# Kernel optimization log

Measured on AMD Instinct MI355X. Metric: run time of the kernel, lower is better.

The kernel has to match this reference:

```python
import jax, jax.numpy as jnp
import numpy as np

N = 50000
EPS = 1e-5


def _layernorm(x, g, b):
    mu = jnp.mean(x, axis=-1, keepdims=True)
    var = jnp.mean((x - mu) ** 2, axis=-1, keepdims=True)
    return (x - mu) * jax.lax.rsqrt(var + EPS) * g + b


def _gcn_conv(x, W, b, src, dst, norm, n):
    # PyG GCNConv: x' = D^{-1/2}(A+I)D^{-1/2} (x W) + b, self-loops already in src/dst
    xw = x @ W                                   # [N, F_out]
    msg = xw[src] * norm[:, None]                # gather + scale, [E+N, F_out]
    return jax.ops.segment_sum(msg, dst, num_segments=n) + b


def _prep_edges(edge_index, n):
    loops = jnp.arange(n, dtype=edge_index.dtype)
    src = jnp.concatenate([edge_index[0], loops])
    dst = jnp.concatenate([edge_index[1], loops])
    deg = jax.ops.segment_sum(jnp.ones(dst.shape[0], jnp.float32), dst, num_segments=n)
    dinv = jnp.where(deg > 0, jax.lax.rsqrt(deg), 0.0)
    norm = dinv[src] * dinv[dst]
    return src, dst, norm


def setup_inputs() -> dict:
    key = jax.random.key(0)
    ks = jax.random.split(key, 8)
    gene, hid, nc = 512, 256, 4
    x = jax.random.normal(ks[0], (N, gene), jnp.float32)
    edge_index = jax.random.randint(ks[1], (2, 1600000), 0, N, dtype=jnp.int64)

    def lin(k, fi, fo):
        return jax.random.normal(k, (fi, fo), jnp.float32) / np.sqrt(fi)

    d = {
        "x": x, "edge_index": edge_index,
        "W1": lin(ks[2], gene, hid), "b1": jnp.zeros(hid, jnp.float32),
        "W2": lin(ks[3], hid, 2 * hid), "b2": jnp.zeros(2 * hid, jnp.float32),
        "W3": lin(ks[4], 2 * hid, hid), "b3": jnp.zeros(hid, jnp.float32),
        "W4": lin(ks[5], hid, hid // 2), "b4": jnp.zeros(hid // 2, jnp.float32),
        "Wc": lin(ks[6], hid // 2, nc), "bc": jnp.zeros(nc, jnp.float32),
        "g1": jnp.ones(hid, jnp.float32), "be1": jnp.zeros(hid, jnp.float32),
        "g2": jnp.ones(2 * hid, jnp.float32), "be2": jnp.zeros(2 * hid, jnp.float32),
        "g3": jnp.ones(hid, jnp.float32), "be3": jnp.zeros(hid, jnp.float32),
        "g4": jnp.ones(hid // 2, jnp.float32), "be4": jnp.zeros(hid // 2, jnp.float32),
    }
    return d


def reference(x, edge_index, W1, b1, W2, b2, W3, b3, W4, b4, Wc, bc,
              g1, be1, g2, be2, g3, be3, g4, be4):
    n = x.shape[0]
    src, dst, norm = _prep_edges(edge_index, n)
    # dropout layers are identity (training=False)
    h1 = jax.nn.elu(_layernorm(_gcn_conv(x, W1, b1, src, dst, norm, n), g1, be1))
    h2 = jax.nn.elu(_layernorm(_gcn_conv(h1, W2, b2, src, dst, norm, n), g2, be2))
    h3 = jax.nn.elu(_layernorm(_gcn_conv(h2, W3, b3, src, dst, norm, n), g3, be3))
    h4_in = h3 + h1
    out_conv = _gcn_conv(h4_in, W4, b4, src, dst, norm, n)
    out_bn = _layernorm(out_conv, g4, be4)
    h = jax.nn.elu(out_bn)
    return (h @ Wc + bc, out_conv, out_bn)
```

## Files before the change

### kernel.cpp

```cpp
#include <hip/hip_runtime.h>
#include <hip/hip_bf16.h>
#include <math.h>

typedef unsigned short u16;
typedef u16 us8 __attribute__((ext_vector_type(8)));
typedef u16 us4 __attribute__((ext_vector_type(4)));
typedef float f32x4 __attribute__((ext_vector_type(4)));
typedef float f32x8 __attribute__((ext_vector_type(8)));
typedef __bf16 bf8 __attribute__((ext_vector_type(8)));

#define SCAN_B 256
#define CH 8192

__device__ __forceinline__ float bf2f(u16 v) {
    unsigned u = ((unsigned)v) << 16;
    return __builtin_bit_cast(float, u);
}
__device__ __forceinline__ u16 f2bf(float f) {
    unsigned u = __builtin_bit_cast(unsigned, f);
    unsigned lsb = (u >> 16) & 1;
    u += 0x7fff + lsb;
    return (u16)(u >> 16);
}
__device__ __forceinline__ void fma8(f32x8& acc, float w, us8 v) {
#pragma unroll
    for (int j = 0; j < 8; j++) acc[j] += w * bf2f(v[j]);
}

__global__ void detect_k(const int* __restrict__ ei, int E,
                         const u16* __restrict__ xraw, int* flag) {
    __shared__ int c_i32, c_f32;
    if (threadIdx.x == 0) { c_i32 = 0; c_f32 = 0; }
    __syncthreads();
    int ne = (E < 4096) ? E : 4096;
    for (int e = threadIdx.x; e < ne; e += blockDim.x)
        if (ei[2 * e + 1] != 0) c_i32 = 1;
    for (int k = threadIdx.x; k < 8192; k += blockDim.x) {
        u16 v = xraw[2 * k];
        int ex = (v >> 7) & 0xFF;
        if (ex >= 0xF0) atomicAdd(&c_f32, 1);
    }
    __syncthreads();
    if (threadIdx.x == 0) {
        flag[0] = (c_i32 == 0) ? 1 : 0;
        flag[1] = (c_f32 >= 4) ? 1 : 0;
    }
}

struct WEnt { const void* s; u16* dst; int K; int Nn; int base; };
struct PEnt { const void* s; int n; int off; };
struct PTab { PEnt e[14]; };

#define GX_CVT 4096

__global__ void megacvt_k(const void* __restrict__ xsrc, u16* __restrict__ xdst,
                          long nq, WEnt e0, WEnt e1, WEnt e2, WEnt e3, int wtotal,
                          PTab tab, float* __restrict__ pbuf,
                          const int* __restrict__ flag, int gw) {
    int f32m = flag[1];
    int bid = blockIdx.x;
    if (bid < GX_CVT) {
        long i0 = (long)bid * blockDim.x + threadIdx.x;
        long stride = (long)GX_CVT * blockDim.x;
        if (f32m) {
            const f32x4* s = (const f32x4*)xsrc;
            for (long i = i0; i < nq; i += stride) {
                f32x4 v = s[i];
                us4 o;
                #pragma unroll
                for (int j = 0; j < 4; j++) o[j] = f2bf(v[j]);
                ((us4*)xdst)[i] = o;
            }
        } else {
            const us4* s = (const us4*)xsrc;
            for (long i = i0; i < nq; i += stride) ((us4*)xdst)[i] = s[i];
        }
    } else if (bid < GX_CVT + gw) {
        int t = (bid - GX_CVT) * blockDim.x + threadIdx.x;
        if (t >= wtotal) return;
        WEnt en = (t >= e3.base) ? e3 : ((t >= e2.base) ? e2 : ((t >= e1.base) ? e1 : e0));
        int li = t - en.base;
        int k = li / en.Nn, nn = li - k * en.Nn;
        u16 b;
        if (f32m) b = f2bf(((const float*)en.s)[li]);
        else      b = ((const u16*)en.s)[li];
        en.dst[nn * en.K + k] = b;
    } else {
        PEnt en = tab.e[bid - GX_CVT - gw];
        for (int i = threadIdx.x; i < en.n; i += blockDim.x) {
            float v = f32m ? ((const float*)en.s)[i] : bf2f(((const u16*)en.s)[i]);
            pbuf[en.off + i] = v;
        }
    }
}

__global__ void histA_k(const int* __restrict__ ei, const int* __restrict__ flag,
                        int* __restrict__ hist, int* __restrict__ counts,
                        int E, int n, int NB, int NBUK, int shiftv) {
    __shared__ int lh[256];
    int blk = blockIdx.x;
    int gi = blk * 256 + threadIdx.x;
    if (gi < n) counts[gi] = 1;
    for (int b = threadIdx.x; b < NBUK; b += 256) lh[b] = 0;
    __syncthreads();
    int e0 = blk * CH;
    int e1 = min(e0 + CH, E);
    int i64 = flag[0];
    for (int e = e0 + threadIdx.x; e < e1; e += 256) {
        int d;
        if (i64) d = (int)((const long long*)ei)[(size_t)E + e];
        else     d = ei[(size_t)E + e];
        int b = ((unsigned)d < (unsigned)n) ? min(d >> shiftv, NBUK - 1) : (NBUK - 1);
        atomicAdd(&lh[b], 1);
    }
    __syncthreads();
    for (int b = threadIdx.x; b < NBUK; b += 256) hist[b * NB + blk] = lh[b];
}

__global__ void scan1_k(const int* __restrict__ counts, int* incl, int* bsum, int n) {
    __shared__ int tmp[SCAN_B];
    int t = threadIdx.x;
    int i = blockIdx.x * SCAN_B + t;
    int v = (i < n) ? counts[i] : 0;
    tmp[t] = v;
    __syncthreads();
    for (int o = 1; o < SCAN_B; o <<= 1) {
        int x = 0;
        if (t >= o) x = tmp[t - o];
        __syncthreads();
        if (t >= o) tmp[t] += x;
        __syncthreads();
    }
    if (i < n) incl[i] = tmp[t];
    if (t == SCAN_B - 1) bsum[blockIdx.x] = tmp[t];
}

__global__ void scan2_k(const int* __restrict__ bsum, int* bscan, int nb) {
    __shared__ int tmp[SCAN_B];
    int t = threadIdx.x;
    tmp[t] = (t < nb) ? bsum[t] : 0;
    __syncthreads();
    for (int o = 1; o < SCAN_B; o <<= 1) {
        int x = 0;
        if (t >= o) x = tmp[t - o];
        __syncthreads();
        if (t >= o) tmp[t] += x;
        __syncthreads();
    }
    bscan[t] = tmp[t];
}

__global__ void scatC_k(const int* __restrict__ ei, const int* __restrict__ flag,
                        const int* __restrict__ histincl, const int* __restrict__ bscan,
                        const int* __restrict__ hist, long long* __restrict__ ebuf,
                        int* __restrict__ counts,
                        int E, int n, int NB, int NBUK, int shiftv) {
    __shared__ int cur[256];
    int blk = blockIdx.x;
    for (int b = threadIdx.x; b < NBUK; b += 256) {
        int fi = b * NB + blk;
        int boff = (fi >= 256) ? bscan[(fi >> 8) - 1] : 0;
        cur[b] = histincl[fi] + boff - hist[fi];
    }
    __syncthreads();
    int e0 = blk * CH;
    int e1 = min(e0 + CH, E);
    int i64 = flag[0];
    for (int e = e0 + threadIdx.x; e < e1; e += 256) {
        int s, d;
        if (i64) {
            const long long* e64 = (const long long*)ei;
            s = (int)e64[e]; d = (int)e64[(size_t)E + e];
        } else {
            s = ei[e]; d = ei[(size_t)E + e];
        }
        int b = ((unsigned)d < (unsigned)n) ? min(d >> shiftv, NBUK - 1) : (NBUK - 1);
        int pos = atomicAdd(&cur[b], 1);
        ebuf[pos] = ((long long)(unsigned)d << 32) | (unsigned)s;
        if ((unsigned)d < (unsigned)n) atomicAdd(&counts[d], 1);
    }
}

__global__ void finCSR_k(const int* __restrict__ incl, const int* __restrict__ bscan,
                         const int* __restrict__ counts, int* __restrict__ rowptr,
                         int* __restrict__ cursor, float* __restrict__ dinv, int n) {
    int i = blockIdx.x * SCAN_B + threadIdx.x;
    if (i < n) {
        int boff = (blockIdx.x > 0) ? bscan[blockIdx.x - 1] : 0;
        int rp_end = incl[i] + boff;
        rowptr[i + 1] = rp_end;
        if (i == 0) rowptr[0] = 0;
        cursor[i] = rp_end - counts[i];
        dinv[i] = rsqrtf((float)counts[i]);
    }
}

__global__ void scatD_k(const long long* __restrict__ ebuf, int* cursor,
                        int* __restrict__ col, int E, int n) {
    int e = blockIdx.x * blockDim.x + threadIdx.x;
    if (e < E) {
        long long pr = ebuf[e];
        int d = (int)(pr >> 32);
        int s = (int)(pr & 0xffffffffLL);
        if ((unsigned)s < (unsigned)n && (unsigned)d < (unsigned)n) {
            int pos = atomicAdd(&cursor[d], 1);
            col[pos] = s;
        }
    } else if (e < E + n) {
        int i = e - E;
        int pos = atomicAdd(&cursor[i], 1);
        col[pos] = i;
    }
}

typedef __attribute__((address_space(1))) const void gas_v;
typedef __attribute__((address_space(3))) void las_v;

__global__ __launch_bounds__(256) void gemm128_k(
    const u16* __restrict__ A, const u16* __restrict__ Bt,
    u16* __restrict__ C, int M, int K, int Nn, int nyv) {
    int nx = (M + 127) >> 7;
    int nfull = nx & ~7;
    int cutoff = nfull * nyv;
    int b = blockIdx.x;
    int bx, by;
    if (b < cutoff) {
        int k = b & 7;
        int q = b >> 3;
        by = q % nyv;
        bx = (q / nyv) * 8 + k;
    } else {
        int r = b - cutoff;
        bx = nfull + r / nyv;
        by = r % nyv;
    }

    __shared__ u16 As[2][128 * 32];
    __shared__ u16 Bs[2][128 * 32];
    int tid = threadIdx.x;
    int wave = tid >> 6;
    int lane = tid & 63;
    int wr = (wave >> 1) * 64;
    int wc = (wave & 1) * 64;
    long row0 = (long)bx * 128;
    int col0 = by * 128;
    int lr = lane >> 2;
    int lc = lane & 3;
    int m = lane & 15;
    int q = lane >> 4;

    long ar0 = row0 + (wave + 0) * 16 + lr;
    long ar1 = row0 + (wave + 4) * 16 + lr;
    if (ar0 > (long)M - 1) ar0 = (long)M - 1;
    if (ar1 > (long)M - 1) ar1 = (long)M - 1;
    const u16* gA0 = A + ar0 * K + lc * 8;
    const u16* gA1 = A + ar1 * K + lc * 8;
    const u16* gB0 = Bt + (size_t)(col0 + (wave + 0) * 16 + lr) * K + lc * 8;
    const u16* gB1 = Bt + (size_t)(col0 + (wave + 4) * 16 + lr) * K + lc * 8;
    int lds0 = (wave + 0) * 512;
    int lds1 = (wave + 4) * 512;

    f32x4 acc[4][4];
    #pragma unroll
    for (int i = 0; i < 4; i++)
        #pragma unroll
        for (int j = 0; j < 4; j++) acc[i][j] = (f32x4){0.f, 0.f, 0.f, 0.f};

    __builtin_amdgcn_global_load_lds((gas_v*)(gA0), (las_v*)&As[0][lds0], 16, 0, 0);
    __builtin_amdgcn_global_load_lds((gas_v*)(gA1), (las_v*)&As[0][lds1], 16, 0, 0);
    __builtin_amdgcn_global_load_lds((gas_v*)(gB0), (las_v*)&Bs[0][lds0], 16, 0, 0);
    __builtin_amdgcn_global_load_lds((gas_v*)(gB1), (las_v*)&Bs[0][lds1], 16, 0, 0);
    __syncthreads();

    int cur = 0;
    for (int k0 = 0; k0 < K; k0 += 32) {
        if (k0 + 32 < K) {
            int nb = cur ^ 1;
            int ko = k0 + 32;
            __builtin_amdgcn_global_load_lds((gas_v*)(gA0 + ko), (las_v*)&As[nb][lds0], 16, 0, 0);
            __builtin_amdgcn_global_load_lds((gas_v*)(gA1 + ko), (las_v*)&As[nb][lds1], 16, 0, 0);
            __builtin_amdgcn_global_load_lds((gas_v*)(gB0 + ko), (las_v*)&Bs[nb][lds0], 16, 0, 0);
            __builtin_amdgcn_global_load_lds((gas_v*)(gB1 + ko), (las_v*)&Bs[nb][lds1], 16, 0, 0);
        }

        us8 av[4], bv[4];
        #pragma unroll
        for (int i = 0; i < 4; i++) {
            av[i] = *(const us8*)&As[cur][(wr + i * 16 + m) * 32 + q * 8];
            bv[i] = *(const us8*)&Bs[cur][(wc + i * 16 + m) * 32 + q * 8];
        }
        #pragma unroll
        for (int i = 0; i < 4; i++) {
            bf8 fa = __builtin_bit_cast(bf8, av[i]);
            #pragma unroll
            for (int j = 0; j < 4; j++) {
                bf8 fb = __builtin_bit_cast(bf8, bv[j]);
                acc[i][j] = __builtin_amdgcn_mfma_f32_16x16x32_bf16(fa, fb, acc[i][j], 0, 0, 0);
            }
        }
        __syncthreads();
        cur ^= 1;
    }

    #pragma unroll
    for (int i = 0; i < 4; i++) {
        #pragma unroll
        for (int r = 0; r < 4; r++) {
            long row = row0 + wr + i * 16 + q * 4 + r;
            if (row < M) {
                #pragma unroll
                for (int j = 0; j < 4; j++)
                    C[row * Nn + col0 + wc + j * 16 + m] = f2bf(acc[i][j][r]);
            }
        }
    }
}

template <int F>
__global__ __launch_bounds__(256) void agg_k(
    const u16* __restrict__ in, const int* __restrict__ rowptr,
    const int* __restrict__ col, const float* __restrict__ dinv,
    const float* __restrict__ bias, const float* __restrict__ gamma,
    const float* __restrict__ beta, u16* __restrict__ out_h,
    const u16* __restrict__ resid, void* __restrict__ final_base,
    const int* __restrict__ flag, const float* __restrict__ Wcf,
    const float* __restrict__ bcf, int nN) {
    int wv = threadIdx.x >> 6;
    int lane = threadIdx.x & 63;
    int i = blockIdx.x * 4 + wv;
    if (i >= nN) return;

    constexpr int rowt = F >> 3;
    constexpr int Gw = 64 / rowt;
    int g = lane / rowt;
    int f0 = (lane & (rowt - 1)) << 3;

    int beg = rowptr[i], end = rowptr[i + 1];
    f32x8 acc = {0, 0, 0, 0, 0, 0, 0, 0}, acc2 = acc;
    int e = beg + g;
    for (; e + Gw < end; e += 2 * Gw) {
        int s0 = col[e], s1 = col[e + Gw];
        s0 = ((unsigned)s0 < (unsigned)nN) ? s0 : 0;
        s1 = ((unsigned)s1 < (unsigned)nN) ? s1 : 0;
        float w0 = dinv[s0], w1 = dinv[s1];
        us8 v0 = *(const us8*)(in + (unsigned)(s0 * F) + f0);
        us8 v1 = *(const us8*)(in + (unsigned)(s1 * F) + f0);
        fma8(acc, w0, v0);
        fma8(acc2, w1, v1);
    }
    if (e < end) {
        int s = col[e];
        s = ((unsigned)s < (unsigned)nN) ? s : 0;
        us8 v = *(const us8*)(in + (unsigned)(s * F) + f0);
        fma8(acc, dinv[s], v);
    }
    #pragma unroll
    for (int j = 0; j < 8; j++) acc[j] += acc2[j];

    #pragma unroll
    for (int o = 32; o >= rowt; o >>= 1) {
        #pragma unroll
        for (int j = 0; j < 8; j++) acc[j] += __shfl_down(acc[j], o);
    }
    bool active = lane < rowt;
    float di = dinv[i];

    if (!bias) {
        if (active) {
            us8 o8;
            #pragma unroll
            for (int j = 0; j < 8; j++) o8[j] = f2bf(di * acc[j]);
            *(us8*)(out_h + (unsigned)(i * F) + f0) = o8;
        }
        return;
    }

    f32x8 accv = {0, 0, 0, 0, 0, 0, 0, 0};
    if (active) {
        #pragma unroll
        for (int j = 0; j < 8; j++) accv[j] = di * acc[j] + bias[f0 + j];
    }
    int f32m = final_base ? flag[1] : 0;
    if (final_base && active) {
        size_t conv_idx = (size_t)nN * 4 + (size_t)i * F + f0;
        if (f32m) {
            #pragma unroll
            for (int j = 0; j < 8; j++) ((float*)final_base)[conv_idx + j] = accv[j];
        } else {
            us8 o8;
            #pragma unroll
            for (int j = 0; j < 8; j++) o8[j] = f2bf(accv[j]);
            *(us8*)((u16*)final_base + conv_idx) = o8;
        }
    }

    float p1 = 0.f, p2 = 0.f;
    #pragma unroll
    for (int j = 0; j < 8; j++) { p1 += accv[j]; p2 += accv[j] * accv[j]; }
    #pragma unroll
    for (int o = rowt >> 1; o >= 1; o >>= 1) {
        p1 += __shfl_xor(p1, o);
        p2 += __shfl_xor(p2, o);
    }
    constexpr float invF = 1.0f / (float)F;
    float mu = p1 * invF;
    float var = fmaxf(p2 * invF - mu * mu, 0.f);
    float rstd = rsqrtf(var + 1e-5f);

    f32x8 h8 = {0, 0, 0, 0, 0, 0, 0, 0};
    if (active) {
        f32x8 y8;
        #pragma unroll
        for (int j = 0; j < 8; j++)
            y8[j] = (accv[j] - mu) * rstd * gamma[f0 + j] + beta[f0 + j];
        if (final_base) {
            size_t bn_idx = (size_t)nN * 4 + (size_t)nN * F + (size_t)i * F + f0;
            if (f32m) {
                #pragma unroll
                for (int j = 0; j < 8; j++) ((float*)final_base)[bn_idx + j] = y8[j];
            } else {
                us8 o8;
                #pragma unroll
                for (int j = 0; j < 8; j++) o8[j] = f2bf(y8[j]);
                *(us8*)((u16*)final_base + bn_idx) = o8;
            }
        }
        #pragma unroll
        for (int j = 0; j < 8; j++) h8[j] = (y8[j] > 0.f) ? y8[j] : expm1f(y8[j]);
        if (resid) {
            us8 r8 = *(const us8*)(resid + (unsigned)(i * F) + f0);
            #pragma unroll
            for (int j = 0; j < 8; j++) h8[j] += bf2f(r8[j]);
        }
        if (out_h) {
            us8 o8;
            #pragma unroll
            for (int j = 0; j < 8; j++) o8[j] = f2bf(h8[j]);
            *(us8*)(out_h + (unsigned)(i * F) + f0) = o8;
        }
    }

    if (Wcf) {
        float s0 = 0.f, s1 = 0.f, s2 = 0.f, s3 = 0.f;
        if (active) {
            #pragma unroll
            for (int j = 0; j < 8; j++) {
                const float* wr = Wcf + (f0 + j) * 4;
                s0 += h8[j] * wr[0];
                s1 += h8[j] * wr[1];
                s2 += h8[j] * wr[2];
                s3 += h8[j] * wr[3];
            }
        }
        #pragma unroll
        for (int o = rowt >> 1; o >= 1; o >>= 1) {
            s0 += __shfl_xor(s0, o);
            s1 += __shfl_xor(s1, o);
            s2 += __shfl_xor(s2, o);
            s3 += __shfl_xor(s3, o);
        }
        if (lane == 0) {
            size_t lidx = (size_t)i * 4;
            if (f32m) {
                ((float*)final_base)[lidx + 0] = s0 + bcf[0];
                ((float*)final_base)[lidx + 1] = s1 + bcf[1];
                ((float*)final_base)[lidx + 2] = s2 + bcf[2];
                ((float*)final_base)[lidx + 3] = s3 + bcf[3];
            } else {
                ((u16*)final_base)[lidx + 0] = f2bf(s0 + bcf[0]);
                ((u16*)final_base)[lidx + 1] = f2bf(s1 + bcf[1]);
                ((u16*)final_base)[lidx + 2] = f2bf(s2 + bcf[2]);
                ((u16*)final_base)[lidx + 3] = f2bf(s3 + bcf[3]);
            }
        }
    }
}

__global__ __launch_bounds__(256) void ln_elu_k(u16* __restrict__ h,
                                                const float* __restrict__ bias,
                                                const float* __restrict__ gamma,
                                                const float* __restrict__ beta, int nN) {
    int wv = threadIdx.x >> 6;
    int lane = threadIdx.x & 63;
    int i = blockIdx.x * 4 + wv;
    if (i >= nN) return;
    int f0 = lane * 8;
    size_t base = (size_t)i * 512 + f0;
    us8 v8 = *(const us8*)(h + base);
    f32x8 v;
    #pragma unroll
    for (int j = 0; j < 8; j++) v[j] = bf2f(v8[j]) + bias[f0 + j];
    float p1 = 0.f, p2 = 0.f;
    #pragma unroll
    for (int j = 0; j < 8; j++) { p1 += v[j]; p2 += v[j] * v[j]; }
    #pragma unroll
    for (int o = 32; o >= 1; o >>= 1) {
        p1 += __shfl_xor(p1, o);
        p2 += __shfl_xor(p2, o);
    }
    const float invF = 1.0f / 512.0f;
    float mu = p1 * invF;
    float var = fmaxf(p2 * invF - mu * mu, 0.f);
    float rstd = rsqrtf(var + 1e-5f);
    us8 o8;
    #pragma unroll
    for (int j = 0; j < 8; j++) {
        float y = (v[j] - mu) * rstd * gamma[f0 + j] + beta[f0 + j];
        y = (y > 0.f) ? y : expm1f(y);
        o8[j] = f2bf(y);
    }
    *(us8*)(h + base) = o8;
}

__global__ void marker_k(float* out) {
    if (threadIdx.x == 0 && blockIdx.x == 0) {
        out[0] = 31337.0f; out[1] = 31337.0f;
    }
}

extern "C" void kernel_launch(void* const* d_in, const int* in_sizes, int n_in,
                              void* d_out, int out_size, void* d_ws, size_t ws_size,
                              hipStream_t stream) {
    const int N = in_sizes[0] / 512;
    const int E = in_sizes[1] / 2;

    const void* x  = d_in[0];
    const int* ei  = (const int*)d_in[1];

    char* p = (char*)d_ws;
    auto alloc = [&](size_t bytes) -> void* {
        void* r = (void*)p;
        p += (bytes + 255) & ~(size_t)255;
        return r;
    };
    int*   flag   = (int*)alloc(256);
    int*   counts = (int*)alloc((size_t)N * 4);
    int*   rowptr = (int*)alloc((size_t)(N + 1) * 4);
    int*   cursor = (int*)alloc((size_t)N * 4);
    int*   incl   = (int*)alloc((size_t)N * 4);
    int*   bsum   = (int*)alloc(256 * 4);
    int*   bscan  = (int*)alloc(256 * 4);
    float* dinv   = (float*)alloc((size_t)N * 4);
    int*   col    = (int*)alloc((size_t)(E + N) * 4);
    float* pbuf   = (float*)alloc(4096 * 4);
    u16* W1t = (u16*)alloc((size_t)512 * 256 * 2);
    u16* W2t = (u16*)alloc((size_t)256 * 512 * 2);
    u16* W3t = (u16*)alloc((size_t)512 * 256 * 2);
    u16* W4t = (u16*)alloc((size_t)256 * 128 * 2);
    u16* bigA = (u16*)alloc((size_t)N * 512 * 2);
    u16* xw   = (u16*)alloc((size_t)N * 256 * 2);
    u16* h1   = (u16*)alloc((size_t)N * 256 * 2);

    size_t needed = (size_t)(p - (char*)d_ws);
    if (needed > ws_size) {
        marker_k<<<1, 64, 0, stream>>>((float*)d_out);
        return;
    }

    u16* xbf = bigA;
    u16* h2  = bigA;

    int shiftv = 8;
    while (((N - 1) >> shiftv) > 255) shiftv++;
    int NBUK = ((N - 1) >> shiftv) + 1;
    int NB_E = (E + CH - 1) / CH;
    int flatlen = NBUK * NB_E;
    int NH = (flatlen + 255) / 256;
    long long* ebuf = (long long*)xw;
    int* hist     = (int*)h1;
    int* histincl = hist + flatlen;

    PTab tab;
    tab.e[0]  = { d_in[3],  256, 0    };
    tab.e[1]  = { d_in[12], 256, 256  };
    tab.e[2]  = { d_in[13], 256, 512  };
    tab.e[3]  = { d_in[5],  512, 768  };
    tab.e[4]  = { d_in[14], 512, 1280 };
    tab.e[5]  = { d_in[15], 512, 1792 };
    tab.e[6]  = { d_in[7],  256, 2304 };
    tab.e[7]  = { d_in[16], 256, 2560 };
    tab.e[8]  = { d_in[17], 256, 2816 };
    tab.e[9]  = { d_in[9],  128, 3072 };
    tab.e[10] = { d_in[18], 128, 3200 };
    tab.e[11] = { d_in[19], 128, 3328 };
    tab.e[12] = { d_in[10], 512, 3456 };
    tab.e[13] = { d_in[11], 4,   3968 };
    float* b1f = pbuf + 0,   *g1f = pbuf + 256,  *be1f = pbuf + 512;
    float* b2f = pbuf + 768, *g2f = pbuf + 1280, *be2f = pbuf + 1792;
    float* b3f = pbuf + 2304,*g3f = pbuf + 2560, *be3f = pbuf + 2816;
    float* b4f = pbuf + 3072,*g4f = pbuf + 3200, *be4f = pbuf + 3328;
    float* Wcf = pbuf + 3456,*bcf = pbuf + 3968;

    int NB = (N + SCAN_B - 1) / SCAN_B;

    detect_k<<<1, 256, 0, stream>>>(ei, E, (const u16*)x, flag);

    {
        WEnt e0 = { d_in[2], W1t, 512, 256, 0 };
        WEnt e1 = { d_in[4], W2t, 256, 512, 512 * 256 };
        WEnt e2 = { d_in[6], W3t, 512, 256, 512 * 256 + 256 * 512 };
        WEnt e3 = { d_in[8], W4t, 256, 128, 512 * 256 * 2 + 256 * 512 };
        int wtotal = 512 * 256 * 2 + 256 * 512 + 256 * 128;
        int gw = (wtotal + 255) / 256;
        megacvt_k<<<GX_CVT + gw + 14, 256, 0, stream>>>(
            x, xbf, (long)N * 512 / 4, e0, e1, e2, e3, wtotal, tab, pbuf, flag, gw);
    }

    histA_k<<<NB_E, 256, 0, stream>>>(ei, flag, hist, counts, E, N, NB_E, NBUK, shiftv);
    scan1_k<<<NH, SCAN_B, 0, stream>>>(hist, histincl, bsum, flatlen);
    scan2_k<<<1, SCAN_B, 0, stream>>>(bsum, bscan, NH);
    scatC_k<<<NB_E, 256, 0, stream>>>(ei, flag, histincl, bscan, hist, ebuf, counts,
                                      E, N, NB_E, NBUK, shiftv);
    scan1_k<<<NB, SCAN_B, 0, stream>>>(counts, incl, bsum, N);
    scan2_k<<<1, SCAN_B, 0, stream>>>(bsum, bscan, NB);
    finCSR_k<<<NB, SCAN_B, 0, stream>>>(incl, bscan, counts, rowptr, cursor, dinv, N);
    scatD_k<<<(E + N + 255) / 256, 256, 0, stream>>>(ebuf, cursor, col, E, N);

    int gx = (N + 127) / 128;
    int ga = (N + 3) / 4;

    gemm128_k<<<gx * 2, 256, 0, stream>>>(xbf, W1t, xw, N, 512, 256, 2);
    agg_k<256><<<ga, 256, 0, stream>>>(xw, rowptr, col, dinv, b1f, g1f, be1f,
                                       h1, nullptr, nullptr, flag, nullptr, nullptr, N);
    agg_k<256><<<ga, 256, 0, stream>>>(h1, rowptr, col, dinv, nullptr, nullptr, nullptr,
                                       xw, nullptr, nullptr, flag, nullptr, nullptr, N);
    gemm128_k<<<gx * 4, 256, 0, stream>>>(xw, W2t, h2, N, 256, 512, 4);
    ln_elu_k<<<ga, 256, 0, stream>>>(h2, b2f, g2f, be2f, N);
    gemm128_k<<<gx * 2, 256, 0, stream>>>(h2, W3t, xw, N, 512, 256, 2);
    agg_k<256><<<ga, 256, 0, stream>>>(xw, rowptr, col, dinv, b3f, g3f, be3f,
                                       h1, h1, nullptr, flag, nullptr, nullptr, N);
    gemm128_k<<<gx * 1, 256, 0, stream>>>(h1, W4t, xw, N, 256, 128, 1);
    agg_k<128><<<ga, 256, 0, stream>>>(xw, rowptr, col, dinv, b4f, g4f, be4f,
                                       nullptr, nullptr, d_out, flag, Wcf, bcf, N);
}
```

Before: 965.7 us.

## Build CSR per destination bucket with shared-memory counting and scatter

Replaces global atomic degree counting and the global-cursor scatter with per-bucket kernels. Each bucket block scans its slice of the bucketed edge buffer, counting degrees and then placing columns using shared-memory atomics over 256-node windows. The aim is to remove contended global atomics and random global cursor traffic. In exchange, each block rereads its bucket slice once per 256-node window, and the order of edges within a row may change.

```diff
diff --git a/kernel.cpp b/kernel.cpp
--- a/kernel.cpp
+++ b/kernel.cpp
@@ -95,12 +95,10 @@
 }
 
 __global__ void histA_k(const int* __restrict__ ei, const int* __restrict__ flag,
-                        int* __restrict__ hist, int* __restrict__ counts,
+                        int* __restrict__ hist,
                         int E, int n, int NB, int NBUK, int shiftv) {
     __shared__ int lh[256];
     int blk = blockIdx.x;
-    int gi = blk * 256 + threadIdx.x;
-    if (gi < n) counts[gi] = 1;
     for (int b = threadIdx.x; b < NBUK; b += 256) lh[b] = 0;
     __syncthreads();
     int e0 = blk * CH;
@@ -153,7 +151,6 @@
 __global__ void scatC_k(const int* __restrict__ ei, const int* __restrict__ flag,
                         const int* __restrict__ histincl, const int* __restrict__ bscan,
                         const int* __restrict__ hist, long long* __restrict__ ebuf,
-                        int* __restrict__ counts,
                         int E, int n, int NB, int NBUK, int shiftv) {
     __shared__ int cur[256];
     int blk = blockIdx.x;
@@ -177,39 +174,103 @@
         int b = ((unsigned)d < (unsigned)n) ? min(d >> shiftv, NBUK - 1) : (NBUK - 1);
         int pos = atomicAdd(&cur[b], 1);
         ebuf[pos] = ((long long)(unsigned)d << 32) | (unsigned)s;
-        if ((unsigned)d < (unsigned)n) atomicAdd(&counts[d], 1);
-    }
-}
-
-__global__ void finCSR_k(const int* __restrict__ incl, const int* __restrict__ bscan,
+    }
+}
+
+__global__ void countS_k(const long long* __restrict__ ebuf,
+                         const int* __restrict__ histincl, const int* __restrict__ bscan,
+                         const int* __restrict__ hist, int* __restrict__ counts,
+                         int E, int n, int NB, int NBUK, int shiftv) {
+    __shared__ int cnt[256];
+    __shared__ int sse[2];
+    int b = blockIdx.x;
+    int t = threadIdx.x;
+    if (t < 2) {
+        int bb = b + t;
+        int v;
+        if (bb >= NBUK) v = E;
+        else {
+            int fi = bb * NB;
+            int boff = (fi >= 256) ? bscan[(fi >> 8) - 1] : 0;
+            v = histincl[fi] + boff - hist[fi];
+        }
+        sse[t] = v;
+    }
+    __syncthreads();
+    int sb = sse[0], se = sse[1];
+    int base = b << shiftv;
+    int W = 1 << shiftv;
+    for (int w0 = 0; w0 < W; w0 += 256) {
+        cnt[t] = 0;
+        __syncthreads();
+        for (int e = sb + t; e < se; e += 256) {
+            int d = (int)(ebuf[e] >> 32);
+            int loc = d - base - w0;
+            if ((unsigned)d < (unsigned)n && (unsigned)loc < 256u)
+                atomicAdd(&cnt[loc], 1);
+        }
+        __syncthreads();
+        int i = base + w0 + t;
+        if (i < n) counts[i] = cnt[t] + 1;
+        __syncthreads();
+    }
+}
+
+__global__ void finCSR_k(const int* __restrict__ nincl, const int* __restrict__ nbscan,
                          const int* __restrict__ counts, int* __restrict__ rowptr,
-                         int* __restrict__ cursor, float* __restrict__ dinv, int n) {
+                         float* __restrict__ dinv, int n) {
     int i = blockIdx.x * SCAN_B + threadIdx.x;
     if (i < n) {
-        int boff = (blockIdx.x > 0) ? bscan[blockIdx.x - 1] : 0;
-        int rp_end = incl[i] + boff;
+        int boff = (blockIdx.x > 0) ? nbscan[blockIdx.x - 1] : 0;
+        int rp_end = nincl[i] + boff;
         rowptr[i + 1] = rp_end;
         if (i == 0) rowptr[0] = 0;
-        cursor[i] = rp_end - counts[i];
         dinv[i] = rsqrtf((float)counts[i]);
     }
 }
 
-__global__ void scatD_k(const long long* __restrict__ ebuf, int* cursor,
-                        int* __restrict__ col, int E, int n) {
-    int e = blockIdx.x * blockDim.x + threadIdx.x;
-    if (e < E) {
-        long long pr = ebuf[e];
-        int d = (int)(pr >> 32);
-        int s = (int)(pr & 0xffffffffLL);
-        if ((unsigned)s < (unsigned)n && (unsigned)d < (unsigned)n) {
-            int pos = atomicAdd(&cursor[d], 1);
-            col[pos] = s;
-        }
-    } else if (e < E + n) {
-        int i = e - E;
-        int pos = atomicAdd(&cursor[i], 1);
-        col[pos] = i;
+__global__ void scatDS_k(const long long* __restrict__ ebuf,
+                         const int* __restrict__ histincl, const int* __restrict__ bscan,
+                         const int* __restrict__ hist, const int* __restrict__ rowptr,
+                         int* __restrict__ col,
+                         int E, int n, int NB, int NBUK, int shiftv) {
+    __shared__ int cur[256];
+    __shared__ int sse[2];
+    int b = blockIdx.x;
+    int t = threadIdx.x;
+    if (t < 2) {
+        int bb = b + t;
+        int v;
+        if (bb >= NBUK) v = E;
+        else {
+            int fi = bb * NB;
+            int boff = (fi >= 256) ? bscan[(fi >> 8) - 1] : 0;
+            v = histincl[fi] + boff - hist[fi];
+        }
+        sse[t] = v;
+    }
+    __syncthreads();
+    int sb = sse[0], se = sse[1];
+    int base = b << shiftv;
+    int W = 1 << shiftv;
+    for (int w0 = 0; w0 < W; w0 += 256) {
+        int node = base + w0 + t;
+        cur[t] = (node < n) ? rowptr[node] : 0;
+        __syncthreads();
+        for (int e = sb + t; e < se; e += 256) {
+            long long pr = ebuf[e];
+            int d = (int)(pr >> 32);
+            int s = (int)(pr & 0xffffffffLL);
+            int loc = d - base - w0;
+            if ((unsigned)d < (unsigned)n && (unsigned)s < (unsigned)n &&
+                (unsigned)loc < 256u) {
+                int pos = atomicAdd(&cur[loc], 1);
+                col[pos] = s;
+            }
+        }
+        __syncthreads();
+        if (node < n) col[cur[t]] = node;
+        __syncthreads();
     }
 }
 
@@ -536,10 +597,11 @@
     int*   flag   = (int*)alloc(256);
     int*   counts = (int*)alloc((size_t)N * 4);
     int*   rowptr = (int*)alloc((size_t)(N + 1) * 4);
-    int*   cursor = (int*)alloc((size_t)N * 4);
     int*   incl   = (int*)alloc((size_t)N * 4);
     int*   bsum   = (int*)alloc(256 * 4);
     int*   bscan  = (int*)alloc(256 * 4);
+    int*   nbsum  = (int*)alloc(256 * 4);
+    int*   nbscan = (int*)alloc(256 * 4);
     float* dinv   = (float*)alloc((size_t)N * 4);
     int*   col    = (int*)alloc((size_t)(E + N) * 4);
     float* pbuf   = (float*)alloc(4096 * 4);
@@ -606,15 +668,18 @@
             x, xbf, (long)N * 512 / 4, e0, e1, e2, e3, wtotal, tab, pbuf, flag, gw);
     }
 
-    histA_k<<<NB_E, 256, 0, stream>>>(ei, flag, hist, counts, E, N, NB_E, NBUK, shiftv);
+    histA_k<<<NB_E, 256, 0, stream>>>(ei, flag, hist, E, N, NB_E, NBUK, shiftv);
     scan1_k<<<NH, SCAN_B, 0, stream>>>(hist, histincl, bsum, flatlen);
     scan2_k<<<1, SCAN_B, 0, stream>>>(bsum, bscan, NH);
-    scatC_k<<<NB_E, 256, 0, stream>>>(ei, flag, histincl, bscan, hist, ebuf, counts,
+    scatC_k<<<NB_E, 256, 0, stream>>>(ei, flag, histincl, bscan, hist, ebuf,
                                       E, N, NB_E, NBUK, shiftv);
-    scan1_k<<<NB, SCAN_B, 0, stream>>>(counts, incl, bsum, N);
-    scan2_k<<<1, SCAN_B, 0, stream>>>(bsum, bscan, NB);
-    finCSR_k<<<NB, SCAN_B, 0, stream>>>(incl, bscan, counts, rowptr, cursor, dinv, N);
-    scatD_k<<<(E + N + 255) / 256, 256, 0, stream>>>(ebuf, cursor, col, E, N);
+    countS_k<<<NBUK, 256, 0, stream>>>(ebuf, histincl, bscan, hist, counts,
+                                       E, N, NB_E, NBUK, shiftv);
+    scan1_k<<<NB, SCAN_B, 0, stream>>>(counts, incl, nbsum, N);
+    scan2_k<<<1, SCAN_B, 0, stream>>>(nbsum, nbscan, NB);
+    finCSR_k<<<NB, SCAN_B, 0, stream>>>(incl, nbscan, counts, rowptr, dinv, N);
+    scatDS_k<<<NBUK, 256, 0, stream>>>(ebuf, histincl, bscan, hist, rowptr, col,
+                                       E, N, NB_E, NBUK, shiftv);
 
     int gx = (N + 127) / 128;
     int ga = (N + 3) / 4;
```

Measured after the change: 898.7 us. -6.9%, faster.
